# Performance work log

Hardware: AMD Instinct MI355X
Metric: run time of the kernel (lower is better)

Reference implementation:

```python
import jax, jax.numpy as jnp
import numpy as np

B, C, H, W = 64, 3, 512, 512


def setup_inputs() -> dict:
    key = jax.random.key(0)
    k1, k2, k3 = jax.random.split(key, 3)
    img = jax.random.normal(k1, (B, C, H, W), dtype=jnp.float32)
    rot = jax.random.normal(k2, (B,), dtype=jnp.float32)          # radians
    trans = jax.random.normal(k3, (B, 2), dtype=jnp.float32) * 0.1
    scale = jnp.ones((B,), dtype=jnp.float32)
    return {"img": img, "rot": rot, "trans": trans, "scale": scale}


def reference(img, rot, trans, scale):
    # Batched equivalent of the per-image loop:
    #   theta = [[cos/s, -sin/s, tx], [sin/s, cos/s, ty]]  (2x3 per image)
    #   grid  = F.affine_grid(theta, img.size())           (align_corners=False)
    #   out   = F.grid_sample(img, grid)                    (bilinear, zeros pad)
    b_, c_, h_, w_ = img.shape
    cs = jnp.cos(rot) / scale
    sn = jnp.sin(rot) / scale

    # Base normalized grid (align_corners=False): x_i = (2i+1)/W - 1
    xs = (2.0 * jnp.arange(w_, dtype=img.dtype) + 1.0) / w_ - 1.0
    ys = (2.0 * jnp.arange(h_, dtype=img.dtype) + 1.0) / h_ - 1.0
    gy, gx = jnp.meshgrid(ys, xs, indexing="ij")  # [H, W]

    # Apply affine: [gx', gy'] = theta @ [gx, gy, 1]
    gx_t = cs[:, None, None] * gx + (-sn)[:, None, None] * gy + trans[:, 0, None, None]
    gy_t = sn[:, None, None] * gx + cs[:, None, None] * gy + trans[:, 1, None, None]

    # Unnormalize (align_corners=False): ix = ((g+1)*W - 1)/2
    ix = ((gx_t + 1.0) * w_ - 1.0) * 0.5
    iy = ((gy_t + 1.0) * h_ - 1.0) * 0.5

    x0 = jnp.floor(ix)
    y0 = jnp.floor(iy)
    wx1 = ix - x0  # frac weights
    wy1 = iy - y0
    x0i = x0.astype(jnp.int32)
    y0i = y0.astype(jnp.int32)

    bidx = jnp.arange(b_)[:, None, None]  # [B,1,1]

    def corner(yi, xi, w):
        valid = (xi >= 0) & (xi < w_) & (yi >= 0) & (yi < h_)
        yc = jnp.clip(yi, 0, h_ - 1)
        xc = jnp.clip(xi, 0, w_ - 1)
        v = img[bidx, :, yc, xc]  # [B,H,W,C] gather
        return v * (w * valid)[..., None]

    out = (
        corner(y0i, x0i, (1.0 - wy1) * (1.0 - wx1))
        + corner(y0i, x0i + 1, (1.0 - wy1) * wx1)
        + corner(y0i + 1, x0i, wy1 * (1.0 - wx1))
        + corner(y0i + 1, x0i + 1, wy1 * wx1)
    )
    return jnp.transpose(out, (0, 3, 1, 2))  # [B,C,H,W]
```

## Files before the change

kernel.cpp:

```cpp
#include <hip/hip_runtime.h>
#include <stdint.h>

#define BB 64
#define CC 3
#define HH 512
#define WW 512
#define TILE 32
#define MAXBH 48
#define MAXBW 52
#define PLST 52

typedef float f32x2 __attribute__((ext_vector_type(2)));
typedef float f32x4 __attribute__((ext_vector_type(4)));

__device__ __forceinline__ void pix2in(float x, float y,
                                       float cs, float sn, float tx, float ty,
                                       float& ix, float& iy)
{
    float gx = (2.0f * x + 1.0f) * (1.0f / (float)WW) - 1.0f;
    float gy = (2.0f * y + 1.0f) * (1.0f / (float)HH) - 1.0f;
    float gxt = cs * gx - sn * gy + tx;
    float gyt = sn * gx + cs * gy + ty;
    ix = ((gxt + 1.0f) * (float)WW - 1.0f) * 0.5f;
    iy = ((gyt + 1.0f) * (float)HH - 1.0f) * 0.5f;
}

__global__ __launch_bounds__(256) void warp_setup(
    const float* __restrict__ rot, const float* __restrict__ trans,
    const float* __restrict__ scale, float* __restrict__ ws)
{
    const int i = blockIdx.x * 256 + threadIdx.x;
    const int b = i >> 8, t = i & 255;
    const float r = rot[b];
    const float inv_s = 1.0f / scale[b];
    const float cs = cosf(r) * inv_s;
    const float sn = sinf(r) * inv_s;
    const float tx = trans[2 * b], ty = trans[2 * b + 1];
    if (t == 0)
        reinterpret_cast<float4*>(ws)[b] = make_float4(cs, sn, tx, ty);

    const int oy0 = (t >> 4) * TILE;
    const int ox0 = (t & 15) * TILE;
    float ixa, iya, ixb, iyb, ixc, iyc, ixd, iyd;
    pix2in((float)ox0,              (float)oy0,              cs, sn, tx, ty, ixa, iya);
    pix2in((float)(ox0 + TILE - 1), (float)oy0,              cs, sn, tx, ty, ixb, iyb);
    pix2in((float)ox0,              (float)(oy0 + TILE - 1), cs, sn, tx, ty, ixc, iyc);
    pix2in((float)(ox0 + TILE - 1), (float)(oy0 + TILE - 1), cs, sn, tx, ty, ixd, iyd);
    const float minix = fminf(fminf(ixa, ixb), fminf(ixc, ixd));
    const float maxix = fmaxf(fmaxf(ixa, ixb), fmaxf(ixc, ixd));
    const float miniy = fminf(fminf(iya, iyb), fminf(iyc, iyd));
    const float maxiy = fmaxf(fmaxf(iya, iyb), fmaxf(iyc, iyd));
    const int bx0 = (int)floorf(minix) - 1;
    const int bx1 = (int)floorf(maxix) + 2;
    const int by0 = (int)floorf(miniy) - 1;
    const int by1 = (int)floorf(maxiy) + 2;
    int bx0c = bx0 & ~3;
    const int bw = bx1 - bx0c + 1;
    const int bh = by1 - by0 + 1;

    const uint32_t fit      = (bw <= MAXBW && bh <= MAXBH) ? 1u : 0u;
    const uint32_t interior = (bx0c >= 0 && bx1 < WW && by0 >= 0 && by1 < HH) ? 1u : 0u;
    const int bx0s = min(max(bx0c, -2048), 2047);
    const int by0s = min(max(by0,  -2048), 2047);
    const int bhs  = min(bh, 63);
    const uint32_t desc = ((uint32_t)bx0s & 0xFFFu)
                        | (((uint32_t)by0s & 0xFFFu) << 12)
                        | ((uint32_t)bhs << 24)
                        | (fit << 30) | (interior << 31);
    reinterpret_cast<uint32_t*>(ws)[256 + i] = desc;
}

template <bool INTERIOR>
__device__ __forceinline__ void compute_store(
    const float* __restrict__ pl, float* __restrict__ outb,
    int tid, int ox0, int oy0, int bx0c, int by0,
    float cs, float sn, float tpx, float tpy, long plane)
{
    const int row = tid >> 4;
    const int xp  = (tid & 15) * 2;
    const int oy  = oy0 + row;
    const int oxb = ox0 + xp;

    float ix0, iy0;
    pix2in((float)oxb, (float)oy, cs, sn, tpx, tpy, ix0, iy0);

    float r0[2], r1[2], r2[2];
    #pragma unroll
    for (int e = 0; e < 2; ++e) {
        const float ix = fmaf((float)e, cs, ix0);
        const float iy = fmaf((float)e, sn, iy0);
        const float x0f = floorf(ix), y0f = floorf(iy);
        const float wx1 = ix - x0f,  wy1 = iy - y0f;
        const float wx0 = 1.0f - wx1, wy0 = 1.0f - wy1;
        const int x0 = (int)x0f, y0 = (int)y0f;

        float w00 = wy0 * wx0, w01 = wy0 * wx1, w10 = wy1 * wx0, w11 = wy1 * wx1;
        if (!INTERIOR) {
            const int x1 = x0 + 1, y1 = y0 + 1;
            const float vx0 = (x0 >= 0 && x0 < WW) ? 1.0f : 0.0f;
            const float vx1 = (x1 >= 0 && x1 < WW) ? 1.0f : 0.0f;
            const float vy0 = (y0 >= 0 && y0 < HH) ? 1.0f : 0.0f;
            const float vy1 = (y1 >= 0 && y1 < HH) ? 1.0f : 0.0f;
            w00 *= vy0 * vx0; w01 *= vy0 * vx1; w10 *= vy1 * vx0; w11 *= vy1 * vx1;
        }

        const int idx = (y0 - by0) * PLST + (x0 - bx0c);
        const float* pb = pl + idx;
        #pragma unroll
        for (int c = 0; c < CC; ++c) {
            const float* pc = pb + c * (MAXBH * PLST);
            const float v00 = pc[0];
            const float v01 = pc[1];
            const float v10 = pc[PLST];
            const float v11 = pc[PLST + 1];
            const float v = w00 * v00 + w01 * v01 + w10 * v10 + w11 * v11;
            if (c == 0) r0[e] = v; else if (c == 1) r1[e] = v; else r2[e] = v;
        }
    }
    const long ob = (long)oy * WW + oxb;
    const f32x2 o0 = {r0[0], r0[1]};
    const f32x2 o1 = {r1[0], r1[1]};
    const f32x2 o2 = {r2[0], r2[1]};
    __builtin_nontemporal_store(o0, reinterpret_cast<f32x2*>(outb + ob));
    __builtin_nontemporal_store(o1, reinterpret_cast<f32x2*>(outb + plane + ob));
    __builtin_nontemporal_store(o2, reinterpret_cast<f32x2*>(outb + 2 * plane + ob));
}

__global__ __launch_bounds__(512) void warp_tiled(
    const float* __restrict__ img, const float* __restrict__ ws,
    float* __restrict__ out)
{
    __shared__ __align__(16) float pl[CC][MAXBH][PLST];

    const int g   = blockIdx.x;
    const int swz = (g & 7) * ((BB * 256) / 8) + (g >> 3);
    const int b   = swz >> 8;
    const int t   = swz & 255;
    const int oy0 = (t >> 4) * TILE;
    const int ox0 = (t & 15) * TILE;

    const float4 p = reinterpret_cast<const float4*>(ws)[b];
    const float cs = p.x, sn = p.y, tpx = p.z, tpy = p.w;
    const uint32_t desc = reinterpret_cast<const uint32_t*>(ws)[256 + swz];
    const int  bx0c     = ((int)(desc << 20)) >> 20;
    const int  by0      = ((int)(desc << 8))  >> 20;
    const int  bh       = (desc >> 24) & 63;
    const bool fit      = (desc >> 30) & 1;
    const bool interior = (desc >> 31) & 1;

    const long plane = (long)HH * WW;
    const float* imb = img + (long)b * CC * plane;
    float* outb      = out + (long)b * CC * plane;
    const int tid = threadIdx.x;

    if (fit) {
        const int q  = tid >> 4;
        const int ql = tid & 15;
        if (ql < 13) {
            const int xb = ql * 4;
            if (interior && (bx0c + 51 < WW)) {
                for (int r = q; r < bh; r += 32) {
                    const float* pr = imb + (long)(by0 + r) * WW + (bx0c + xb);
                    const f32x4 a = *reinterpret_cast<const f32x4*>(pr);
                    const f32x4 bv = *reinterpret_cast<const f32x4*>(pr + plane);
                    const f32x4 cv = *reinterpret_cast<const f32x4*>(pr + 2 * plane);
                    *reinterpret_cast<f32x4*>(&pl[0][r][xb]) = a;
                    *reinterpret_cast<f32x4*>(&pl[1][r][xb]) = bv;
                    *reinterpret_cast<f32x4*>(&pl[2][r][xb]) = cv;
                }
            } else {
                for (int r = q; r < bh; r += 32) {
                    const int grow = by0 + r;
                    const bool rowok = (grow >= 0) && (grow < HH);
                    const float* pr = imb + (long)grow * WW;
                    f32x4 a = {0.f, 0.f, 0.f, 0.f}, bv = a, cv = a;
                    #pragma unroll
                    for (int k = 0; k < 4; ++k) {
                        const int gcol = bx0c + xb + k;
                        if (rowok && gcol >= 0 && gcol < WW) {
                            a[k]  = pr[gcol];
                            bv[k] = pr[(long)gcol + plane];
                            cv[k] = pr[(long)gcol + 2 * plane];
                        }
                    }
                    *reinterpret_cast<f32x4*>(&pl[0][r][xb]) = a;
                    *reinterpret_cast<f32x4*>(&pl[1][r][xb]) = bv;
                    *reinterpret_cast<f32x4*>(&pl[2][r][xb]) = cv;
                }
            }
        }
        __syncthreads();

        if (interior)
            compute_store<true >(&pl[0][0][0], outb, tid, ox0, oy0, bx0c, by0, cs, sn, tpx, tpy, plane);
        else
            compute_store<false>(&pl[0][0][0], outb, tid, ox0, oy0, bx0c, by0, cs, sn, tpx, tpy, plane);
    } else {
        #pragma unroll
        for (int k = 0; k < 2; ++k) {
            const int pidx = tid + k * 512;
            const int py = pidx >> 5;
            const int px = pidx & 31;
            const int ox = ox0 + px, oy = oy0 + py;

            float ix, iy;
            pix2in((float)ox, (float)oy, cs, sn, tpx, tpy, ix, iy);
            const float x0f = floorf(ix), y0f = floorf(iy);
            const float wx1 = ix - x0f,  wy1 = iy - y0f;
            const int x0 = (int)x0f, y0 = (int)y0f;
            const int x1 = x0 + 1,  y1 = y0 + 1;

            const float vx0 = (x0 >= 0 && x0 < WW) ? 1.0f : 0.0f;
            const float vx1 = (x1 >= 0 && x1 < WW) ? 1.0f : 0.0f;
            const float vy0 = (y0 >= 0 && y0 < HH) ? 1.0f : 0.0f;
            const float vy1 = (y1 >= 0 && y1 < HH) ? 1.0f : 0.0f;

            const int x0c = min(max(x0, 0), WW - 1);
            const int x1c = min(max(x1, 0), WW - 1);
            const int y0c = min(max(y0, 0), HH - 1);
            const int y1c = min(max(y1, 0), HH - 1);

            const float w00 = (1.0f - wy1) * (1.0f - wx1) * vy0 * vx0;
            const float w01 = (1.0f - wy1) * wx1          * vy0 * vx1;
            const float w10 = wy1          * (1.0f - wx1) * vy1 * vx0;
            const float w11 = wy1          * wx1          * vy1 * vx1;

            const int o00 = y0c * WW + x0c, o01 = y0c * WW + x1c;
            const int o10 = y1c * WW + x0c, o11 = y1c * WW + x1c;
            const int ob = oy * WW + ox;
            #pragma unroll
            for (int c = 0; c < CC; ++c) {
                const float* pc = imb + (long)c * plane;
                const float v = w00 * pc[o00] + w01 * pc[o01]
                              + w10 * pc[o10] + w11 * pc[o11];
                __builtin_nontemporal_store(v, &outb[(long)c * plane + ob]);
            }
        }
    }
}

extern "C" void kernel_launch(void* const* d_in, const int* in_sizes, int n_in,
                              void* d_out, int out_size, void* d_ws, size_t ws_size,
                              hipStream_t stream) {
    const float* img   = (const float*)d_in[0];
    const float* rot   = (const float*)d_in[1];
    const float* trans = (const float*)d_in[2];
    const float* scale = (const float*)d_in[3];
    float* out = (float*)d_out;
    float* ws  = (float*)d_ws;

    warp_setup<<<dim3(BB), 256, 0, stream>>>(rot, trans, scale, ws);
    warp_tiled<<<dim3(BB * 256), 512, 0, stream>>>(img, ws, out);
}
```

Before: 67.68 us.

## Process four tiles per block with register-staged prefetch of the next tile's patch

Each block now handles four consecutive 32x32 output tiles instead of one, and the grid shrinks to a quarter of its former size. While the current tile is computed from LDS, the next tile's input patch is loaded into registers and written to LDS after a barrier. The aim is to hide global-load latency behind the bilinear compute and stores, and to amortize block launch cost. In exchange it uses more registers for staging, adds extra barriers, and runs fewer blocks, which may reduce occupancy and the memory-level parallelism the hardware gets from many resident blocks.

After: 84.87 us. 25.4% more time.

```diff
diff --git a/kernel.cpp b/kernel.cpp
--- a/kernel.cpp
+++ b/kernel.cpp
@@ -9,6 +9,7 @@
 #define MAXBH 48
 #define MAXBW 52
 #define PLST 52
+#define NT 4
 
 typedef float f32x2 __attribute__((ext_vector_type(2)));
 typedef float f32x4 __attribute__((ext_vector_type(4)));
@@ -70,6 +71,77 @@
     reinterpret_cast<uint32_t*>(ws)[256 + i] = desc;
 }
 
+struct Stage { f32x4 a0, b0, c0, a1, b1, c1; };
+
+__device__ __forceinline__ Stage stage_load(uint32_t desc, const float* __restrict__ imb,
+                                            long plane, int q, int ql)
+{
+    Stage s = {};
+    const bool fit = (desc >> 30) & 1;
+    if (!fit || ql >= 13) return s;
+    const int  bx0c     = ((int)(desc << 20)) >> 20;
+    const int  by0      = ((int)(desc << 8))  >> 20;
+    const int  bh       = (desc >> 24) & 63;
+    const bool interior = (desc >> 31) & 1;
+    const int  xb       = ql * 4;
+
+    if (interior && (bx0c + 51 < WW)) {
+        const float* pr = imb + (long)(by0 + q) * WW + (bx0c + xb);
+        if (q < bh) {
+            s.a0 = *reinterpret_cast<const f32x4*>(pr);
+            s.b0 = *reinterpret_cast<const f32x4*>(pr + plane);
+            s.c0 = *reinterpret_cast<const f32x4*>(pr + 2 * plane);
+        }
+        if (q + 32 < bh) {
+            const float* p2 = pr + 32 * WW;
+            s.a1 = *reinterpret_cast<const f32x4*>(p2);
+            s.b1 = *reinterpret_cast<const f32x4*>(p2 + plane);
+            s.c1 = *reinterpret_cast<const f32x4*>(p2 + 2 * plane);
+        }
+    } else {
+        #pragma unroll
+        for (int h = 0; h < 2; ++h) {
+            const int r = q + h * 32;
+            if (r >= bh) continue;
+            const int grow = by0 + r;
+            const bool rowok = (grow >= 0) && (grow < HH);
+            const float* pr = imb + (long)grow * WW;
+            f32x4 a = {0.f,0.f,0.f,0.f}, bv = a, cv = a;
+            #pragma unroll
+            for (int k = 0; k < 4; ++k) {
+                const int gcol = bx0c + xb + k;
+                if (rowok && gcol >= 0 && gcol < WW) {
+                    a[k]  = pr[gcol];
+                    bv[k] = pr[(long)gcol + plane];
+                    cv[k] = pr[(long)gcol + 2 * plane];
+                }
+            }
+            if (h == 0) { s.a0 = a; s.b0 = bv; s.c0 = cv; }
+            else        { s.a1 = a; s.b1 = bv; s.c1 = cv; }
+        }
+    }
+    return s;
+}
+
+__device__ __forceinline__ void lds_write(const Stage& s, uint32_t desc,
+                                          float* __restrict__ pl, int q, int ql)
+{
+    const bool fit = (desc >> 30) & 1;
+    if (!fit || ql >= 13) return;
+    const int bh = (desc >> 24) & 63;
+    const int xb = ql * 4;
+    if (q < bh) {
+        *reinterpret_cast<f32x4*>(pl + 0 * (MAXBH * PLST) + q * PLST + xb) = s.a0;
+        *reinterpret_cast<f32x4*>(pl + 1 * (MAXBH * PLST) + q * PLST + xb) = s.b0;
+        *reinterpret_cast<f32x4*>(pl + 2 * (MAXBH * PLST) + q * PLST + xb) = s.c0;
+    }
+    if (q + 32 < bh) {
+        *reinterpret_cast<f32x4*>(pl + 0 * (MAXBH * PLST) + (q + 32) * PLST + xb) = s.a1;
+        *reinterpret_cast<f32x4*>(pl + 1 * (MAXBH * PLST) + (q + 32) * PLST + xb) = s.b1;
+        *reinterpret_cast<f32x4*>(pl + 2 * (MAXBH * PLST) + (q + 32) * PLST + xb) = s.c1;
+    }
+}
+
 template <bool INTERIOR>
 __device__ __forceinline__ void compute_store(
     const float* __restrict__ pl, float* __restrict__ outb,
@@ -109,11 +181,8 @@
         #pragma unroll
         for (int c = 0; c < CC; ++c) {
             const float* pc = pb + c * (MAXBH * PLST);
-            const float v00 = pc[0];
-            const float v01 = pc[1];
-            const float v10 = pc[PLST];
-            const float v11 = pc[PLST + 1];
-            const float v = w00 * v00 + w01 * v01 + w10 * v10 + w11 * v11;
+            const float v = w00 * pc[0] + w01 * pc[1]
+                          + w10 * pc[PLST] + w11 * pc[PLST + 1];
             if (c == 0) r0[e] = v; else if (c == 1) r1[e] = v; else r2[e] = v;
         }
     }
@@ -126,116 +195,116 @@
     __builtin_nontemporal_store(o2, reinterpret_cast<f32x2*>(outb + 2 * plane + ob));
 }
 
+__device__ __forceinline__ void fallback_tile(
+    const float* __restrict__ imb, float* __restrict__ outb,
+    int tid, int ox0, int oy0,
+    float cs, float sn, float tpx, float tpy, long plane)
+{
+    #pragma unroll
+    for (int k = 0; k < 2; ++k) {
+        const int pidx = tid + k * 512;
+        const int py = pidx >> 5;
+        const int px = pidx & 31;
+        const int ox = ox0 + px, oy = oy0 + py;
+
+        float ix, iy;
+        pix2in((float)ox, (float)oy, cs, sn, tpx, tpy, ix, iy);
+        const float x0f = floorf(ix), y0f = floorf(iy);
+        const float wx1 = ix - x0f,  wy1 = iy - y0f;
+        const int x0 = (int)x0f, y0 = (int)y0f;
+        const int x1 = x0 + 1,  y1 = y0 + 1;
+
+        const float vx0 = (x0 >= 0 && x0 < WW) ? 1.0f : 0.0f;
+        const float vx1 = (x1 >= 0 && x1 < WW) ? 1.0f : 0.0f;
+        const float vy0 = (y0 >= 0 && y0 < HH) ? 1.0f : 0.0f;
+        const float vy1 = (y1 >= 0 && y1 < HH) ? 1.0f : 0.0f;
+
+        const int x0c = min(max(x0, 0), WW - 1);
+        const int x1c = min(max(x1, 0), WW - 1);
+        const int y0c = min(max(y0, 0), HH - 1);
+        const int y1c = min(max(y1, 0), HH - 1);
+
+        const float w00 = (1.0f - wy1) * (1.0f - wx1) * vy0 * vx0;
+        const float w01 = (1.0f - wy1) * wx1          * vy0 * vx1;
+        const float w10 = wy1          * (1.0f - wx1) * vy1 * vx0;
+        const float w11 = wy1          * wx1          * vy1 * vx1;
+
+        const int o00 = y0c * WW + x0c, o01 = y0c * WW + x1c;
+        const int o10 = y1c * WW + x0c, o11 = y1c * WW + x1c;
+        const int ob = oy * WW + ox;
+        #pragma unroll
+        for (int c = 0; c < CC; ++c) {
+            const float* pc = imb + (long)c * plane;
+            const float v = w00 * pc[o00] + w01 * pc[o01]
+                          + w10 * pc[o10] + w11 * pc[o11];
+            __builtin_nontemporal_store(v, &outb[(long)c * plane + ob]);
+        }
+    }
+}
+
 __global__ __launch_bounds__(512) void warp_tiled(
     const float* __restrict__ img, const float* __restrict__ ws,
     float* __restrict__ out)
 {
     __shared__ __align__(16) float pl[CC][MAXBH][PLST];
 
-    const int g   = blockIdx.x;
-    const int swz = (g & 7) * ((BB * 256) / 8) + (g >> 3);
-    const int b   = swz >> 8;
-    const int t   = swz & 255;
-    const int oy0 = (t >> 4) * TILE;
-    const int ox0 = (t & 15) * TILE;
+    const int g    = blockIdx.x;
+    const int swzb = (g & 7) * ((BB * 64) / 8) + (g >> 3);
+    const int b    = swzb >> 6;
+    const int blk  = swzb & 63;
+    const int ty   = blk >> 2;
+    const int qx   = (blk & 3) * NT;
+    const int oy0  = ty * TILE;
 
     const float4 p = reinterpret_cast<const float4*>(ws)[b];
     const float cs = p.x, sn = p.y, tpx = p.z, tpy = p.w;
-    const uint32_t desc = reinterpret_cast<const uint32_t*>(ws)[256 + swz];
-    const int  bx0c     = ((int)(desc << 20)) >> 20;
-    const int  by0      = ((int)(desc << 8))  >> 20;
-    const int  bh       = (desc >> 24) & 63;
-    const bool fit      = (desc >> 30) & 1;
-    const bool interior = (desc >> 31) & 1;
+    const uint32_t* dptr = reinterpret_cast<const uint32_t*>(ws) + 256 + b * 256 + ty * 16 + qx;
 
     const long plane = (long)HH * WW;
     const float* imb = img + (long)b * CC * plane;
     float* outb      = out + (long)b * CC * plane;
     const int tid = threadIdx.x;
-
-    if (fit) {
-        const int q  = tid >> 4;
-        const int ql = tid & 15;
-        if (ql < 13) {
-            const int xb = ql * 4;
-            if (interior && (bx0c + 51 < WW)) {
-                for (int r = q; r < bh; r += 32) {
-                    const float* pr = imb + (long)(by0 + r) * WW + (bx0c + xb);
-                    const f32x4 a = *reinterpret_cast<const f32x4*>(pr);
-                    const f32x4 bv = *reinterpret_cast<const f32x4*>(pr + plane);
-                    const f32x4 cv = *reinterpret_cast<const f32x4*>(pr + 2 * plane);
-                    *reinterpret_cast<f32x4*>(&pl[0][r][xb]) = a;
-                    *reinterpret_cast<f32x4*>(&pl[1][r][xb]) = bv;
-                    *reinterpret_cast<f32x4*>(&pl[2][r][xb]) = cv;
-                }
-            } else {
-                for (int r = q; r < bh; r += 32) {
-                    const int grow = by0 + r;
-                    const bool rowok = (grow >= 0) && (grow < HH);
-                    const float* pr = imb + (long)grow * WW;
-                    f32x4 a = {0.f, 0.f, 0.f, 0.f}, bv = a, cv = a;
-                    #pragma unroll
-                    for (int k = 0; k < 4; ++k) {
-                        const int gcol = bx0c + xb + k;
-                        if (rowok && gcol >= 0 && gcol < WW) {
-                            a[k]  = pr[gcol];
-                            bv[k] = pr[(long)gcol + plane];
-                            cv[k] = pr[(long)gcol + 2 * plane];
-                        }
-                    }
-                    *reinterpret_cast<f32x4*>(&pl[0][r][xb]) = a;
-                    *reinterpret_cast<f32x4*>(&pl[1][r][xb]) = bv;
-                    *reinterpret_cast<f32x4*>(&pl[2][r][xb]) = cv;
-                }
-            }
+    const int q  = tid >> 4;
+    const int ql = tid & 15;
+
+    uint32_t dcur = dptr[0];
+    {
+        Stage s0 = stage_load(dcur, imb, plane, q, ql);
+        lds_write(s0, dcur, &pl[0][0][0], q, ql);
+    }
+    __syncthreads();
+
+    #pragma unroll
+    for (int tt = 0; tt < NT; ++tt) {
+        const int ox0 = (qx + tt) * TILE;
+
+        uint32_t dnext = 0;
+        Stage sn_;
+        if (tt + 1 < NT) {
+            dnext = dptr[tt + 1];
+            sn_ = stage_load(dnext, imb, plane, q, ql);
+        }
+
+        const int  bx0c     = ((int)(dcur << 20)) >> 20;
+        const int  by0      = ((int)(dcur << 8))  >> 20;
+        const bool fit      = (dcur >> 30) & 1;
+        const bool interior = (dcur >> 31) & 1;
+
+        if (fit) {
+            if (interior)
+                compute_store<true >(&pl[0][0][0], outb, tid, ox0, oy0, bx0c, by0, cs, sn, tpx, tpy, plane);
+            else
+                compute_store<false>(&pl[0][0][0], outb, tid, ox0, oy0, bx0c, by0, cs, sn, tpx, tpy, plane);
+        } else {
+            fallback_tile(imb, outb, tid, ox0, oy0, cs, sn, tpx, tpy, plane);
         }
         __syncthreads();
 
-        if (interior)
-            compute_store<true >(&pl[0][0][0], outb, tid, ox0, oy0, bx0c, by0, cs, sn, tpx, tpy, plane);
-        else
-            compute_store<false>(&pl[0][0][0], outb, tid, ox0, oy0, bx0c, by0, cs, sn, tpx, tpy, plane);
-    } else {
-        #pragma unroll
-        for (int k = 0; k < 2; ++k) {
-            const int pidx = tid + k * 512;
-            const int py = pidx >> 5;
-            const int px = pidx & 31;
-            const int ox = ox0 + px, oy = oy0 + py;
-
-            float ix, iy;
-            pix2in((float)ox, (float)oy, cs, sn, tpx, tpy, ix, iy);
-            const float x0f = floorf(ix), y0f = floorf(iy);
-            const float wx1 = ix - x0f,  wy1 = iy - y0f;
-            const int x0 = (int)x0f, y0 = (int)y0f;
-            const int x1 = x0 + 1,  y1 = y0 + 1;
-
-            const float vx0 = (x0 >= 0 && x0 < WW) ? 1.0f : 0.0f;
-            const float vx1 = (x1 >= 0 && x1 < WW) ? 1.0f : 0.0f;
-            const float vy0 = (y0 >= 0 && y0 < HH) ? 1.0f : 0.0f;
-            const float vy1 = (y1 >= 0 && y1 < HH) ? 1.0f : 0.0f;
-
-            const int x0c = min(max(x0, 0), WW - 1);
-            const int x1c = min(max(x1, 0), WW - 1);
-            const int y0c = min(max(y0, 0), HH - 1);
-            const int y1c = min(max(y1, 0), HH - 1);
-
-            const float w00 = (1.0f - wy1) * (1.0f - wx1) * vy0 * vx0;
-            const float w01 = (1.0f - wy1) * wx1          * vy0 * vx1;
-            const float w10 = wy1          * (1.0f - wx1) * vy1 * vx0;
-            const float w11 = wy1          * wx1          * vy1 * vx1;
-
-            const int o00 = y0c * WW + x0c, o01 = y0c * WW + x1c;
-            const int o10 = y1c * WW + x0c, o11 = y1c * WW + x1c;
-            const int ob = oy * WW + ox;
-            #pragma unroll
-            for (int c = 0; c < CC; ++c) {
-                const float* pc = imb + (long)c * plane;
-                const float v = w00 * pc[o00] + w01 * pc[o01]
-                              + w10 * pc[o10] + w11 * pc[o11];
-                __builtin_nontemporal_store(v, &outb[(long)c * plane + ob]);
-            }
-        }
+        if (tt + 1 < NT) {
+            lds_write(sn_, dnext, &pl[0][0][0], q, ql);
+            dcur = dnext;
+        }
+        __syncthreads();
     }
 }
 
@@ -250,5 +319,5 @@
     float* ws  = (float*)d_ws;
 
     warp_setup<<<dim3(BB), 256, 0, stream>>>(rot, trans, scale, ws);
-    warp_tiled<<<dim3(BB * 256), 512, 0, stream>>>(img, ws, out);
-}
+    warp_tiled<<<dim3(BB * 64), 512, 0, stream>>>(img, ws, out);
+}
```
